# Optimization experiments

Measured on AMD Instinct MI355X. Metric: run time of the kernel, lower is better.

The kernel has to match this reference:

```python
import jax, jax.numpy as jnp
import numpy as np

B, Q, F, D, H = 16384, 1024, 2, 5, 4  # batch, n_qubits, n_features, depth, heads


def setup_inputs() -> dict:
    key = jax.random.key(0)
    ks = iter(jax.random.split(key, 16))
    def rnd(shape, s=0.02):
        return jax.random.normal(next(ks), shape, dtype=jnp.float32) * s
    return {
        "x": jax.random.normal(next(ks), (B, F), dtype=jnp.float32),
        # amplitude_encoder: Linear(F,4Q) -> LN -> GELU -> Linear(4Q,2Q) -> LN -> Tanh -> Linear(2Q,Q)
        "amp_W1": rnd((4 * Q, F)), "amp_b1": jnp.zeros((4 * Q,), jnp.float32),
        "amp_g1": jnp.ones((4 * Q,), jnp.float32), "amp_be1": jnp.zeros((4 * Q,), jnp.float32),
        "amp_W2": rnd((2 * Q, 4 * Q)), "amp_b2": jnp.zeros((2 * Q,), jnp.float32),
        "amp_g2": jnp.ones((2 * Q,), jnp.float32), "amp_be2": jnp.zeros((2 * Q,), jnp.float32),
        "amp_W3": rnd((Q, 2 * Q)), "amp_b3": jnp.zeros((Q,), jnp.float32),
        # phase_encoder: Linear(F,2Q) -> LN -> SiLU -> Linear(2Q,Q) -> Tanh
        "ph_W1": rnd((2 * Q, F)), "ph_b1": jnp.zeros((2 * Q,), jnp.float32),
        "ph_g1": jnp.ones((2 * Q,), jnp.float32), "ph_be1": jnp.zeros((2 * Q,), jnp.float32),
        "ph_W2": rnd((Q, 2 * Q)), "ph_b2": jnp.zeros((Q,), jnp.float32),
        # rotation parameters (depth, Q, 3); only the last depth slice survives the overwrite loop
        "rot_freq": jax.random.normal(next(ks), (D, Q, 3), dtype=jnp.float32),
        "rot_phase": jax.random.normal(next(ks), (D, Q, 3), dtype=jnp.float32),
        # MultiheadAttention(Q, 4 heads)
        "attn_in_w": rnd((3 * Q, Q)), "attn_in_b": jnp.zeros((3 * Q,), jnp.float32),
        "attn_out_w": rnd((Q, Q)), "attn_out_b": jnp.zeros((Q,), jnp.float32),
    }


def _ln(x, g, b):
    m = jnp.mean(x, -1, keepdims=True)
    v = jnp.mean((x - m) ** 2, -1, keepdims=True)
    return (x - m) * jax.lax.rsqrt(v + 1e-5) * g + b


def reference(x, amp_W1, amp_b1, amp_g1, amp_be1, amp_W2, amp_b2, amp_g2, amp_be2,
              amp_W3, amp_b3, ph_W1, ph_b1, ph_g1, ph_be1, ph_W2, ph_b2,
              rot_freq, rot_phase, attn_in_w, attn_in_b, attn_out_w, attn_out_b):
    # amplitude encoder (Dropout is identity in eval mode)
    h = jax.nn.gelu(_ln(x @ amp_W1.T + amp_b1, amp_g1, amp_be1), approximate=False)
    h = jnp.tanh(_ln(h @ amp_W2.T + amp_b2, amp_g2, amp_be2))
    amp = h @ amp_W3.T + amp_b3                      # (B, Q)
    # phase encoder
    p = jax.nn.silu(_ln(x @ ph_W1.T + ph_b1, ph_g1, ph_be1))
    phase = jnp.tanh(p @ ph_W2.T + ph_b2)            # (B, Q)
    # multiscale conv branch: n_features=2 < min kernel size 3 => skipped, combined_conv = 0
    # depth loop overwrites quantum_state each iteration => only depth index D-1 matters
    rx = jnp.sin(amp * rot_freq[-1, :, 0] + rot_phase[-1, :, 0])
    ry = jnp.cos(phase * rot_freq[-1, :, 1] + rot_phase[-1, :, 1])
    rz = jnp.broadcast_to(jnp.tanh(rot_phase[-1, :, 2]), rx.shape)  # tanh(0*f + p)
    qs = (rx + ry + rz) / 3.0                        # (B, Q)
    # MultiheadAttention with seq_len == 1: softmax over a single key is exactly 1,
    # so attended output == V projection regardless of Q/K.
    qkv = qs @ attn_in_w.T + attn_in_b               # (B, 3Q)
    v = qkv[:, 2 * Q:]                               # (B, Q)
    return v @ attn_out_w.T + attn_out_b
```

## Files before the change

kernel.cpp:

```cpp
#include <hip/hip_runtime.h>

using bf16x8 = __attribute__((ext_vector_type(8))) __bf16;
using u16x8  = __attribute__((ext_vector_type(8))) unsigned short;
using f32x4  = __attribute__((ext_vector_type(4))) float;

__device__ __forceinline__ unsigned short f2bf(float f){
  unsigned int u = __float_as_uint(f);
  u += 0x7fffu + ((u >> 16) & 1u);
  return (unsigned short)(u >> 16);
}
__device__ __forceinline__ float bf2f(unsigned short h){
  return __uint_as_float(((unsigned int)h) << 16);
}

__global__ __launch_bounds__(256) void cvt_bf16(const float* __restrict__ s,
                                                unsigned short* __restrict__ d, int n){
  int i = blockIdx.x * 256 + threadIdx.x;
  if (i < n) d[i] = f2bf(s[i]);
}

__global__ __launch_bounds__(256) void ln_stats_kernel(
    const float* __restrict__ W, const float* __restrict__ b, int n,
    float* __restrict__ out)
{
  __shared__ float red[9][256];
  const int tid = threadIdx.x;
  float a[9] = {0.f,0.f,0.f,0.f,0.f,0.f,0.f,0.f,0.f};
  for (int j = tid; j < n; j += 256){
    float w0 = W[2*j], w1 = W[2*j+1], bb = b[j];
    a[0] += w0;      a[1] += w1;      a[2] += bb;
    a[3] += w0*w0;   a[4] += w1*w1;   a[5] += bb*bb;
    a[6] += w0*w1;   a[7] += w0*bb;   a[8] += w1*bb;
  }
#pragma unroll
  for (int k = 0; k < 9; k++) red[k][tid] = a[k];
  __syncthreads();
  for (int s = 128; s > 0; s >>= 1){
    if (tid < s){
#pragma unroll
      for (int k = 0; k < 9; k++) red[k][tid] += red[k][tid + s];
    }
    __syncthreads();
  }
  if (tid < 9) out[tid] = red[tid][0] / (float)n;
}

__global__ __launch_bounds__(256) void front_amp_kernel(
    const float* __restrict__ x,
    const float* __restrict__ W1, const float* __restrict__ b1,
    const float* __restrict__ g1, const float* __restrict__ be1,
    const float* __restrict__ st,
    unsigned short* __restrict__ h)
{
  const int row = blockIdx.x;
  const int tid = threadIdx.x;
  const float x0 = x[row * 2 + 0];
  const float x1 = x[row * 2 + 1];
  const float m   = x0 * st[0] + x1 * st[1] + st[2];
  const float e2  = x0*x0*st[3] + x1*x1*st[4] + st[5]
                  + 2.0f*(x0*x1*st[6] + x0*st[7] + x1*st[8]);
  const float inv = rsqrtf(e2 - m * m + 1e-5f);

  const f32x4* W4 = (const f32x4*)(W1 + (size_t)tid * 32);
#pragma unroll
  for (int i8 = 0; i8 < 2; i8++){
    u16x8 o;
#pragma unroll
    for (int q = 0; q < 2; q++){
      f32x4 wa = W4[i8 * 4 + q * 2];
      f32x4 wb = W4[i8 * 4 + q * 2 + 1];
      f32x4 b4 = *(const f32x4*)(b1  + tid * 16 + i8 * 8 + q * 4);
      f32x4 g4 = *(const f32x4*)(g1  + tid * 16 + i8 * 8 + q * 4);
      f32x4 e4 = *(const f32x4*)(be1 + tid * 16 + i8 * 8 + q * 4);
      float vv[4];
      vv[0] = x0 * wa[0] + x1 * wa[1] + b4[0];
      vv[1] = x0 * wa[2] + x1 * wa[3] + b4[1];
      vv[2] = x0 * wb[0] + x1 * wb[1] + b4[2];
      vv[3] = x0 * wb[2] + x1 * wb[3] + b4[3];
#pragma unroll
      for (int t = 0; t < 4; t++){
        float y = (vv[t] - m) * inv * g4[t] + e4[t];
        float ge = 0.5f * y * (1.0f + erff(y * 0.70710678118654752f));
        o[q * 4 + t] = f2bf(ge);
      }
    }
    *(u16x8*)&h[(size_t)row * 4096 + tid * 16 + i8 * 8] = o;
  }
}

__global__ __launch_bounds__(256) void front_ph_kernel(
    const float* __restrict__ x,
    const float* __restrict__ W1, const float* __restrict__ b1,
    const float* __restrict__ g1, const float* __restrict__ be1,
    const float* __restrict__ st,
    unsigned short* __restrict__ p)
{
  const int row = blockIdx.x;
  const int tid = threadIdx.x;
  const float x0 = x[row * 2 + 0];
  const float x1 = x[row * 2 + 1];
  const float m   = x0 * st[0] + x1 * st[1] + st[2];
  const float e2  = x0*x0*st[3] + x1*x1*st[4] + st[5]
                  + 2.0f*(x0*x1*st[6] + x0*st[7] + x1*st[8]);
  const float inv = rsqrtf(e2 - m * m + 1e-5f);

  const f32x4* W4 = (const f32x4*)(W1 + (size_t)tid * 16);
  u16x8 o;
#pragma unroll
  for (int q = 0; q < 2; q++){
    f32x4 wa = W4[q * 2];
    f32x4 wb = W4[q * 2 + 1];
    f32x4 b4 = *(const f32x4*)(b1  + tid * 8 + q * 4);
    f32x4 g4 = *(const f32x4*)(g1  + tid * 8 + q * 4);
    f32x4 e4 = *(const f32x4*)(be1 + tid * 8 + q * 4);
    float vv[4];
    vv[0] = x0 * wa[0] + x1 * wa[1] + b4[0];
    vv[1] = x0 * wa[2] + x1 * wa[3] + b4[1];
    vv[2] = x0 * wb[0] + x1 * wb[1] + b4[2];
    vv[3] = x0 * wb[2] + x1 * wb[3] + b4[3];
#pragma unroll
    for (int t = 0; t < 4; t++){
      float y = (vv[t] - m) * inv * g4[t] + e4[t];
      float si = y / (1.0f + expf(-y));
      o[q * 4 + t] = f2bf(si);
    }
  }
  *(u16x8*)&p[(size_t)row * 2048 + tid * 8] = o;
}

__global__ __launch_bounds__(256) void ln_tanh_kernel(
    unsigned short* __restrict__ c, const float* __restrict__ g,
    const float* __restrict__ be)
{
  __shared__ float partial[8];
  const size_t base = (size_t)blockIdx.x * 2048;
  const int tid = threadIdx.x;
  u16x8 cv = *(const u16x8*)&c[base + tid * 8];
  float v[8];
  float sum = 0.f, sq = 0.f;
#pragma unroll
  for (int k = 0; k < 8; k++){
    float t = bf2f(cv[k]);
    v[k] = t; sum += t; sq += t * t;
  }
#pragma unroll
  for (int off = 32; off > 0; off >>= 1){
    sum += __shfl_xor(sum, off);
    sq  += __shfl_xor(sq,  off);
  }
  const int wv = tid >> 6;
  if ((tid & 63) == 0){ partial[wv * 2] = sum; partial[wv * 2 + 1] = sq; }
  __syncthreads();
  const float ts = partial[0] + partial[2] + partial[4] + partial[6];
  const float tq = partial[1] + partial[3] + partial[5] + partial[7];
  const float mean = ts * (1.0f / 2048.0f);
  const float inv  = rsqrtf(tq * (1.0f / 2048.0f) - mean * mean + 1e-5f);
  {
    f32x4 ga = *(const f32x4*)(g  + tid * 8);
    f32x4 gb = *(const f32x4*)(g  + tid * 8 + 4);
    f32x4 ba = *(const f32x4*)(be + tid * 8);
    f32x4 bb = *(const f32x4*)(be + tid * 8 + 4);
    u16x8 o;
#pragma unroll
    for (int k = 0; k < 8; k++){
      float gk = (k < 4) ? ga[k] : gb[k - 4];
      float bk = (k < 4) ? ba[k] : bb[k - 4];
      float y = (v[k] - mean) * inv * gk + bk;
      o[k] = f2bf(tanhf(y));
    }
    *(u16x8*)&c[base + tid * 8] = o;
  }
}


#define WAITV4() asm volatile("s_waitcnt vmcnt(4)" ::: "memory")
#define WAITV8() asm volatile("s_waitcnt vmcnt(8)" ::: "memory")
#define WAITV0() asm volatile("s_waitcnt vmcnt(0)" ::: "memory")

template<int EPI>
__global__ __launch_bounds__(512, 2) void gemm_bt(
    const unsigned short* __restrict__ A, const unsigned short* __restrict__ B,
    void* __restrict__ outp, int M, int N, int K, int nT,
    const float* __restrict__ bias,
    const float* __restrict__ aux0, const float* __restrict__ aux1,
    const unsigned short* __restrict__ aux2)
{
  __shared__ __align__(16) char smem_raw[131072];
  unsigned short* S = (unsigned short*)smem_raw;

  const int tid  = threadIdx.x;
  const int wave = tid >> 6, lane = tid & 63;
  const int wm = wave >> 1, wn = wave & 1;
  const int lm = lane & 15, lq = lane >> 4;

  int lid = blockIdx.x;
  {
    const int nwg = gridDim.x;
    if ((nwg & 7) == 0) lid = (lid & 7) * (nwg >> 3) + (lid >> 3);
  }
  const int m0 = (lid / nT) * 256, n0 = (lid % nT) * 256;

  f32x4 acc[4][8];
#pragma unroll
  for (int i = 0; i < 4; i++)
#pragma unroll
    for (int j = 0; j < 8; j++) acc[i][j] = (f32x4){0.f, 0.f, 0.f, 0.f};

  const int lr = lane >> 2;
  const int lc = (((lane & 3) ^ ((lr >> 1) & 3)) << 3);
  const unsigned short* gA = A + (size_t)(m0 + wave * 32 + lr) * K + lc;
  const unsigned short* gB = B + (size_t)(n0 + wave * 32 + lr) * K + lc;
  const size_t rowK16 = (size_t)16 * K;

  auto stage = [&](int buf){
    unsigned short* lA = S + buf * 16384 + wave * 1024;
    unsigned short* lB = lA + 8192;
    __builtin_amdgcn_global_load_lds(
        (const __attribute__((address_space(1))) void*)gA,
        (__attribute__((address_space(3))) void*)lA, 16, 0, 0);
    __builtin_amdgcn_global_load_lds(
        (const __attribute__((address_space(1))) void*)(gA + rowK16),
        (__attribute__((address_space(3))) void*)(lA + 512), 16, 0, 0);
    __builtin_amdgcn_global_load_lds(
        (const __attribute__((address_space(1))) void*)gB,
        (__attribute__((address_space(3))) void*)lB, 16, 0, 0);
    __builtin_amdgcn_global_load_lds(
        (const __attribute__((address_space(1))) void*)(gB + rowK16),
        (__attribute__((address_space(3))) void*)(lB + 512), 16, 0, 0);
    gA += 32; gB += 32;
  };

  auto readA = [&](int buf, bf16x8* af){
    const unsigned short* sA = S + buf * 16384;
#pragma unroll
    for (int q = 0; q < 4; q++){
      const int r = wm * 64 + q * 16 + lm;
      af[q] = *(const bf16x8*)&sA[r * 32 + ((lq ^ ((r >> 1) & 3)) << 3)];
    }
  };
  auto readB = [&](int buf, bf16x8* bfr){
    const unsigned short* sB = S + buf * 16384 + 8192;
#pragma unroll
    for (int q = 0; q < 8; q++){
      const int r = wn * 128 + q * 16 + lm;
      bfr[q] = *(const bf16x8*)&sB[r * 32 + ((lq ^ ((r >> 1) & 3)) << 3)];
    }
  };

  auto mfmaAll = [&](const bf16x8* af, const bf16x8* bfr){
    __builtin_amdgcn_s_setprio(1);
#pragma unroll
    for (int i = 0; i < 4; i++)
#pragma unroll
      for (int j = 0; j < 8; j++)
        acc[i][j] = __builtin_amdgcn_mfma_f32_16x16x32_bf16(af[i], bfr[j], acc[i][j], 0, 0, 0);
    __builtin_amdgcn_s_setprio(0);
  };

  const int nTk = K >> 5;
  bf16x8 af[4], bfA[8], bfB[8];
  stage(0); stage(1); stage(2);
  WAITV8();
  __builtin_amdgcn_s_barrier();
  readB(0, bfA);
  for (int t = 0; t < nTk; t += 2){
    if (t + 2 < nTk) WAITV4(); else WAITV0();
    __builtin_amdgcn_s_barrier();
    if (t + 3 < nTk) stage((t + 3) & 3);
    readA(t & 3, af);
    readB((t + 1) & 3, bfB);
    __builtin_amdgcn_sched_barrier(0);
    mfmaAll(af, bfA);
    if (t + 2 < nTk){
      if (t + 3 < nTk) WAITV4(); else WAITV0();
    }
    __builtin_amdgcn_s_barrier();
    if (t + 4 < nTk) stage((t + 4) & 3);
    readA((t + 1) & 3, af);
    if (t + 2 < nTk) readB((t + 2) & 3, bfA);
    __builtin_amdgcn_sched_barrier(0);
    mfmaAll(af, bfB);
  }

  __syncthreads();
  float* ew = (float*)smem_raw + wave * 2112;

#pragma unroll
  for (int i = 0; i < 4; i++){
#pragma unroll
    for (int j = 0; j < 8; j++){
      const int col = n0 + wn * 128 + j * 16 + lm;
      float bcol = bias[col];
      float f0 = 0.f, p0 = 0.f, rzv = 0.f;
      if constexpr (EPI == 1){
        f0 = aux0[3 * col]; p0 = aux1[3 * col]; rzv = tanhf(aux1[3 * col + 2]);
      }
      if constexpr (EPI == 2){
        f0 = aux0[3 * col + 1]; p0 = aux1[3 * col + 1];
      }
#pragma unroll
      for (int r = 0; r < 4; r++){
        const float val = acc[i][j][r];
        float pre;
        if constexpr (EPI == 0 || EPI == 3)      pre = val + bcol;
        else if constexpr (EPI == 1)             pre = sinf((val + bcol) * f0 + p0) + rzv;
        else                                     pre = cosf(tanhf(val + bcol) * f0 + p0);
        ew[(lq * 4 + r) * 132 + j * 16 + lm] = pre;
      }
    }
    if constexpr (EPI != 3){
#pragma unroll
      for (int s = 0; s < 4; s++){
        const int lrow = 4 * s + lq;
        const int grow = m0 + wm * 64 + i * 16 + lrow;
        const float* src = ew + lrow * 132 + lm * 8;
        f32x4 v0 = *(const f32x4*)(src);
        f32x4 v1 = *(const f32x4*)(src + 4);
        const size_t gidx = (size_t)grow * N + n0 + wn * 128 + lm * 8;
        u16x8 o;
        if constexpr (EPI == 1){
          u16x8 ry8 = *(const u16x8*)&aux2[gidx];
#pragma unroll
          for (int t = 0; t < 4; t++){
            o[t]     = f2bf((v0[t] + bf2f(ry8[t]))     * (1.0f / 3.0f));
            o[t + 4] = f2bf((v1[t] + bf2f(ry8[t + 4])) * (1.0f / 3.0f));
          }
        } else {
#pragma unroll
          for (int t = 0; t < 4; t++){
            o[t] = f2bf(v0[t]); o[t + 4] = f2bf(v1[t]);
          }
        }
        *(u16x8*)&((unsigned short*)outp)[gidx] = o;
      }
    } else {
#pragma unroll
      for (int s = 0; s < 8; s++){
        const int lrow = 2 * s + (lane >> 5);
        const int grow = m0 + wm * 64 + i * 16 + lrow;
        const int lcol = (lane & 31) * 4;
        f32x4 v = *(const f32x4*)(ew + lrow * 132 + lcol);
        *(f32x4*)&((float*)outp)[(size_t)grow * N + n0 + wn * 128 + lcol] = v;
      }
    }
  }
}

extern "C" void kernel_launch(void* const* d_in, const int* in_sizes, int n_in,
                              void* d_out, int out_size, void* d_ws, size_t ws_size,
                              hipStream_t stream)
{
  const float* x    = (const float*)d_in[0];
  const float* aW1  = (const float*)d_in[1];
  const float* ab1  = (const float*)d_in[2];
  const float* ag1  = (const float*)d_in[3];
  const float* abe1 = (const float*)d_in[4];
  const float* aW2  = (const float*)d_in[5];
  const float* ab2  = (const float*)d_in[6];
  const float* ag2  = (const float*)d_in[7];
  const float* abe2 = (const float*)d_in[8];
  const float* aW3  = (const float*)d_in[9];
  const float* ab3  = (const float*)d_in[10];
  const float* pW1  = (const float*)d_in[11];
  const float* pb1  = (const float*)d_in[12];
  const float* pg1  = (const float*)d_in[13];
  const float* pbe1 = (const float*)d_in[14];
  const float* pW2  = (const float*)d_in[15];
  const float* pb2  = (const float*)d_in[16];
  const float* rfreq  = (const float*)d_in[17];
  const float* rphase = (const float*)d_in[18];
  const float* aiw  = (const float*)d_in[19];
  const float* aib  = (const float*)d_in[20];
  const float* aow  = (const float*)d_in[21];
  const float* aob  = (const float*)d_in[22];

  const int B = 16384, Q = 1024;

  char* ws = (char*)d_ws;
  size_t off = 0;
  auto alloc = [&](size_t bytes) -> char* {
    char* ptr = ws + off; off += (bytes + 255) & ~(size_t)255; return ptr;
  };
  unsigned short* Wb2  = (unsigned short*)alloc((size_t)2 * Q * 4 * Q * 2);
  unsigned short* Wb3  = (unsigned short*)alloc((size_t)Q * 2 * Q * 2);
  unsigned short* PWb2 = (unsigned short*)alloc((size_t)Q * 2 * Q * 2);
  unsigned short* WVb  = (unsigned short*)alloc((size_t)Q * Q * 2);
  unsigned short* WOb  = (unsigned short*)alloc((size_t)Q * Q * 2);
  float* stA = (float*)alloc(64);
  float* stP = (float*)alloc(64);
  unsigned short* R1   = (unsigned short*)alloc((size_t)B * 4 * Q * 2);
  unsigned short* ry   = (unsigned short*)alloc((size_t)B * Q * 2);

  unsigned short* p  = R1;
  unsigned short* h  = R1;
  unsigned short* qs = R1;
  unsigned short* v  = R1 + (size_t)B * Q;
  unsigned short* c2 = (unsigned short*)d_out;

  cvt_bf16<<<(2*Q*4*Q + 255) / 256, 256, 0, stream>>>(aW2, Wb2, 2*Q*4*Q);
  cvt_bf16<<<(Q*2*Q + 255) / 256, 256, 0, stream>>>(aW3, Wb3, Q*2*Q);
  cvt_bf16<<<(Q*2*Q + 255) / 256, 256, 0, stream>>>(pW2, PWb2, Q*2*Q);
  cvt_bf16<<<(Q*Q + 255) / 256, 256, 0, stream>>>(aiw + (size_t)2*Q*Q, WVb, Q*Q);
  cvt_bf16<<<(Q*Q + 255) / 256, 256, 0, stream>>>(aow, WOb, Q*Q);

  ln_stats_kernel<<<1, 256, 0, stream>>>(pW1, pb1, 2*Q, stP);
  ln_stats_kernel<<<1, 256, 0, stream>>>(aW1, ab1, 4*Q, stA);

  const float* rf4 = rfreq  + (size_t)4 * Q * 3;
  const float* rp4 = rphase + (size_t)4 * Q * 3;

  const int mT = B / 256;
  const int nT1 = 2 * Q / 256;
  const int nTq = Q / 256;

  front_ph_kernel<<<B, 256, 0, stream>>>(x, pW1, pb1, pg1, pbe1, stP, p);
  gemm_bt<2><<<nTq * mT, 512, 0, stream>>>(p, PWb2, ry, B, Q, 2*Q, nTq,
                                           pb2, rf4, rp4, nullptr);

  front_amp_kernel<<<B, 256, 0, stream>>>(x, aW1, ab1, ag1, abe1, stA, h);
  gemm_bt<0><<<nT1 * mT, 512, 0, stream>>>(h, Wb2, c2, B, 2*Q, 4*Q, nT1,
                                           ab2, nullptr, nullptr, nullptr);
  ln_tanh_kernel<<<B, 256, 0, stream>>>(c2, ag2, abe2);

  gemm_bt<1><<<nTq * mT, 512, 0, stream>>>(c2, Wb3, qs, B, Q, 2*Q, nTq,
                                           ab3, rf4, rp4, ry);
  gemm_bt<0><<<nTq * mT, 512, 0, stream>>>(qs, WVb, v, B, Q, Q, nTq,
                                           aib + 2*Q, nullptr, nullptr, nullptr);
  gemm_bt<3><<<nTq * mT, 512, 0, stream>>>(v, WOb, d_out, B, Q, Q, nTq,
                                           aob, nullptr, nullptr, nullptr);
}
```

Baseline: 971.2 us.

## Shrink GEMM tiles to 128x128 with 256 threads and simple double buffering

Reduces the GEMM block tile from 256x256 (512 threads, 4-stage LDS pipeline with split-phase register prefetch) to 128x128 (256 threads, 2-stage LDS ring that waits on all loads every k-step). LDS per block drops from 128KB to 32KB and the launch bound allows 4 blocks per CU, trading per-block arithmetic intensity and deep prefetch for more concurrent blocks and a larger grid. Risks include more global/L2 traffic per FLOP and exposed load latency from the full vmcnt(0) wait each iteration. The epilogue indexing is adjusted to the smaller tile.

```diff
diff --git a/kernel.cpp b/kernel.cpp
--- a/kernel.cpp
+++ b/kernel.cpp
@@ -173,19 +173,17 @@
 }
 
 
-#define WAITV4() asm volatile("s_waitcnt vmcnt(4)" ::: "memory")
-#define WAITV8() asm volatile("s_waitcnt vmcnt(8)" ::: "memory")
 #define WAITV0() asm volatile("s_waitcnt vmcnt(0)" ::: "memory")
 
 template<int EPI>
-__global__ __launch_bounds__(512, 2) void gemm_bt(
+__global__ __launch_bounds__(256, 4) void gemm_bt(
     const unsigned short* __restrict__ A, const unsigned short* __restrict__ B,
     void* __restrict__ outp, int M, int N, int K, int nT,
     const float* __restrict__ bias,
     const float* __restrict__ aux0, const float* __restrict__ aux1,
     const unsigned short* __restrict__ aux2)
 {
-  __shared__ __align__(16) char smem_raw[131072];
+  __shared__ __align__(16) char smem_raw[32768];
   unsigned short* S = (unsigned short*)smem_raw;
 
   const int tid  = threadIdx.x;
@@ -198,13 +196,13 @@
     const int nwg = gridDim.x;
     if ((nwg & 7) == 0) lid = (lid & 7) * (nwg >> 3) + (lid >> 3);
   }
-  const int m0 = (lid / nT) * 256, n0 = (lid % nT) * 256;
-
-  f32x4 acc[4][8];
+  const int m0 = (lid / nT) * 128, n0 = (lid % nT) * 128;
+
+  f32x4 acc[4][4];
 #pragma unroll
   for (int i = 0; i < 4; i++)
 #pragma unroll
-    for (int j = 0; j < 8; j++) acc[i][j] = (f32x4){0.f, 0.f, 0.f, 0.f};
+    for (int j = 0; j < 4; j++) acc[i][j] = (f32x4){0.f, 0.f, 0.f, 0.f};
 
   const int lr = lane >> 2;
   const int lc = (((lane & 3) ^ ((lr >> 1) & 3)) << 3);
@@ -213,8 +211,8 @@
   const size_t rowK16 = (size_t)16 * K;
 
   auto stage = [&](int buf){
-    unsigned short* lA = S + buf * 16384 + wave * 1024;
-    unsigned short* lB = lA + 8192;
+    unsigned short* lA = S + buf * 8192 + wave * 1024;
+    unsigned short* lB = lA + 4096;
     __builtin_amdgcn_global_load_lds(
         (const __attribute__((address_space(1))) void*)gA,
         (__attribute__((address_space(3))) void*)lA, 16, 0, 0);
@@ -231,65 +229,50 @@
   };
 
   auto readA = [&](int buf, bf16x8* af){
-    const unsigned short* sA = S + buf * 16384;
+    const unsigned short* sA = S + buf * 8192;
 #pragma unroll
     for (int q = 0; q < 4; q++){
       const int r = wm * 64 + q * 16 + lm;
       af[q] = *(const bf16x8*)&sA[r * 32 + ((lq ^ ((r >> 1) & 3)) << 3)];
     }
   };
-  auto readB = [&](int buf, bf16x8* bfr){
-    const unsigned short* sB = S + buf * 16384 + 8192;
-#pragma unroll
-    for (int q = 0; q < 8; q++){
-      const int r = wn * 128 + q * 16 + lm;
-      bfr[q] = *(const bf16x8*)&sB[r * 32 + ((lq ^ ((r >> 1) & 3)) << 3)];
+  auto readB = [&](int buf, bf16x8* bf){
+    const unsigned short* sB = S + buf * 8192 + 4096;
+#pragma unroll
+    for (int q = 0; q < 4; q++){
+      const int r = wn * 64 + q * 16 + lm;
+      bf[q] = *(const bf16x8*)&sB[r * 32 + ((lq ^ ((r >> 1) & 3)) << 3)];
     }
   };
 
-  auto mfmaAll = [&](const bf16x8* af, const bf16x8* bfr){
+  const int nTk = K >> 5;
+  bf16x8 af[4], bf[4];
+  stage(0);
+  WAITV0();
+  __builtin_amdgcn_s_barrier();
+  for (int t = 0; t < nTk; ++t){
+    if (t + 1 < nTk) stage((t + 1) & 1);
+    readA(t & 1, af);
+    readB(t & 1, bf);
     __builtin_amdgcn_s_setprio(1);
 #pragma unroll
     for (int i = 0; i < 4; i++)
 #pragma unroll
-      for (int j = 0; j < 8; j++)
-        acc[i][j] = __builtin_amdgcn_mfma_f32_16x16x32_bf16(af[i], bfr[j], acc[i][j], 0, 0, 0);
+      for (int j = 0; j < 4; j++)
+        acc[i][j] = __builtin_amdgcn_mfma_f32_16x16x32_bf16(af[i], bf[j], acc[i][j], 0, 0, 0);
     __builtin_amdgcn_s_setprio(0);
-  };
-
-  const int nTk = K >> 5;
-  bf16x8 af[4], bfA[8], bfB[8];
-  stage(0); stage(1); stage(2);
-  WAITV8();
-  __builtin_amdgcn_s_barrier();
-  readB(0, bfA);
-  for (int t = 0; t < nTk; t += 2){
-    if (t + 2 < nTk) WAITV4(); else WAITV0();
+    WAITV0();
     __builtin_amdgcn_s_barrier();
-    if (t + 3 < nTk) stage((t + 3) & 3);
-    readA(t & 3, af);
-    readB((t + 1) & 3, bfB);
-    __builtin_amdgcn_sched_barrier(0);
-    mfmaAll(af, bfA);
-    if (t + 2 < nTk){
-      if (t + 3 < nTk) WAITV4(); else WAITV0();
-    }
-    __builtin_amdgcn_s_barrier();
-    if (t + 4 < nTk) stage((t + 4) & 3);
-    readA((t + 1) & 3, af);
-    if (t + 2 < nTk) readB((t + 2) & 3, bfA);
-    __builtin_amdgcn_sched_barrier(0);
-    mfmaAll(af, bfB);
   }
 
   __syncthreads();
-  float* ew = (float*)smem_raw + wave * 2112;
+  float* ew = (float*)smem_raw + wave * 1088;
 
 #pragma unroll
   for (int i = 0; i < 4; i++){
 #pragma unroll
-    for (int j = 0; j < 8; j++){
-      const int col = n0 + wn * 128 + j * 16 + lm;
+    for (int j = 0; j < 4; j++){
+      const int col = n0 + wn * 64 + j * 16 + lm;
       float bcol = bias[col];
       float f0 = 0.f, p0 = 0.f, rzv = 0.f;
       if constexpr (EPI == 1){
@@ -305,18 +288,19 @@
         if constexpr (EPI == 0 || EPI == 3)      pre = val + bcol;
         else if constexpr (EPI == 1)             pre = sinf((val + bcol) * f0 + p0) + rzv;
         else                                     pre = cosf(tanhf(val + bcol) * f0 + p0);
-        ew[(lq * 4 + r) * 132 + j * 16 + lm] = pre;
+        ew[(lq * 4 + r) * 68 + j * 16 + lm] = pre;
       }
     }
     if constexpr (EPI != 3){
 #pragma unroll
-      for (int s = 0; s < 4; s++){
-        const int lrow = 4 * s + lq;
+      for (int s = 0; s < 2; s++){
+        const int lrow = s * 8 + (lane >> 3);
         const int grow = m0 + wm * 64 + i * 16 + lrow;
-        const float* src = ew + lrow * 132 + lm * 8;
+        const int lcol = (lane & 7) * 8;
+        const float* src = ew + lrow * 68 + lcol;
         f32x4 v0 = *(const f32x4*)(src);
         f32x4 v1 = *(const f32x4*)(src + 4);
-        const size_t gidx = (size_t)grow * N + n0 + wn * 128 + lm * 8;
+        const size_t gidx = (size_t)grow * N + n0 + wn * 64 + lcol;
         u16x8 o;
         if constexpr (EPI == 1){
           u16x8 ry8 = *(const u16x8*)&aux2[gidx];
@@ -335,12 +319,12 @@
       }
     } else {
 #pragma unroll
-      for (int s = 0; s < 8; s++){
-        const int lrow = 2 * s + (lane >> 5);
+      for (int s = 0; s < 4; s++){
+        const int lrow = s * 4 + (lane >> 4);
         const int grow = m0 + wm * 64 + i * 16 + lrow;
-        const int lcol = (lane & 31) * 4;
-        f32x4 v = *(const f32x4*)(ew + lrow * 132 + lcol);
-        *(f32x4*)&((float*)outp)[(size_t)grow * N + n0 + wn * 128 + lcol] = v;
+        const int lcol = (lane & 15) * 4;
+        f32x4 v = *(const f32x4*)(ew + lrow * 68 + lcol);
+        *(f32x4*)&((float*)outp)[(size_t)grow * N + n0 + wn * 64 + lcol] = v;
       }
     }
   }
@@ -409,23 +393,23 @@
   const float* rf4 = rfreq  + (size_t)4 * Q * 3;
   const float* rp4 = rphase + (size_t)4 * Q * 3;
 
-  const int mT = B / 256;
-  const int nT1 = 2 * Q / 256;
-  const int nTq = Q / 256;
+  const int mT = B / 128;
+  const int nT1 = 2 * Q / 128;
+  const int nTq = Q / 128;
 
   front_ph_kernel<<<B, 256, 0, stream>>>(x, pW1, pb1, pg1, pbe1, stP, p);
-  gemm_bt<2><<<nTq * mT, 512, 0, stream>>>(p, PWb2, ry, B, Q, 2*Q, nTq,
+  gemm_bt<2><<<nTq * mT, 256, 0, stream>>>(p, PWb2, ry, B, Q, 2*Q, nTq,
                                            pb2, rf4, rp4, nullptr);
 
   front_amp_kernel<<<B, 256, 0, stream>>>(x, aW1, ab1, ag1, abe1, stA, h);
-  gemm_bt<0><<<nT1 * mT, 512, 0, stream>>>(h, Wb2, c2, B, 2*Q, 4*Q, nT1,
+  gemm_bt<0><<<nT1 * mT, 256, 0, stream>>>(h, Wb2, c2, B, 2*Q, 4*Q, nT1,
                                            ab2, nullptr, nullptr, nullptr);
   ln_tanh_kernel<<<B, 256, 0, stream>>>(c2, ag2, abe2);
 
-  gemm_bt<1><<<nTq * mT, 512, 0, stream>>>(c2, Wb3, qs, B, Q, 2*Q, nTq,
+  gemm_bt<1><<<nTq * mT, 256, 0, stream>>>(c2, Wb3, qs, B, Q, 2*Q, nTq,
                                            ab3, rf4, rp4, ry);
-  gemm_bt<0><<<nTq * mT, 512, 0, stream>>>(qs, WVb, v, B, Q, Q, nTq,
+  gemm_bt<0><<<nTq * mT, 256, 0, stream>>>(qs, WVb, v, B, Q, Q, nTq,
                                            aib + 2*Q, nullptr, nullptr, nullptr);
-  gemm_bt<3><<<nTq * mT, 512, 0, stream>>>(v, WOb, d_out, B, Q, Q, nTq,
+  gemm_bt<3><<<nTq * mT, 256, 0, stream>>>(v, WOb, d_out, B, Q, Q, nTq,
                                            aob, nullptr, nullptr, nullptr);
 }
```

Measured after the change: 1.034 ms. 6.5% more time.
